# Optimization experiments

Hardware: AMD Instinct MI355X
Metric: run time of the kernel (lower is better)

Reference implementation:

```python
import jax, jax.numpy as jnp
import numpy as np

B, T, D = 2, 2048, 1024
F_DIM = 4096
E = 8


def setup_inputs() -> dict:
    key = jax.random.key(0)
    ks = jax.random.split(key, 6)
    x = jax.random.normal(ks[0], (B, T, D), dtype=jnp.float32)
    Wr = jax.random.normal(ks[1], (E, D), dtype=jnp.float32) * 0.02  # router weight [E, D]
    W1 = jax.random.normal(ks[2], (E, F_DIM, D), dtype=jnp.float32) * 0.02  # per-expert Linear(D->F) weights
    b1 = jnp.zeros((E, F_DIM), dtype=jnp.float32)
    W2 = jax.random.normal(ks[3], (E, D, F_DIM), dtype=jnp.float32) * 0.02  # per-expert Linear(F->D) weights
    b2 = jnp.zeros((E, D), dtype=jnp.float32)
    return {"x": x, "Wr": Wr, "W1": W1, "b1": b1, "W2": W2, "b2": b2, "top_k": 2}


def reference(x, Wr, W1, b1, W2, b2, top_k):
    # router scores: [b, t, E]
    scores = jnp.einsum('btd,ed->bte', x, Wr)
    topk_vals, topk_idx = jax.lax.top_k(scores, top_k)  # [b, t, k]
    # Dense compute over all experts (E is small); grouped-GEMM equivalent of the
    # original per-token loop. hidden: [b, t, E, F]
    h = jax.nn.relu(jnp.einsum('btd,efd->btef', x, W1) + b1)
    all_out = jnp.einsum('btef,edf->bted', h, W2) + b2  # [b, t, E, D]
    # gather the top-k experts' outputs per token: [b, t, k, D]
    gathered = jnp.take_along_axis(all_out, topk_idx[..., None], axis=2)
    # FAITHFUL to source: softmax over the sequence dim (dim=-1 of [b, t]),
    # applied independently per top-k slot.
    weight = jax.nn.softmax(topk_vals, axis=1)  # [b, t, k]
    out = jnp.sum(weight[..., None] * gathered, axis=2)  # [b, t, D]
    return out
```

## Files before the change

kernel.cpp:

```cpp
#include <hip/hip_runtime.h>
#include <stdint.h>

typedef short bf16x8 __attribute__((ext_vector_type(8)));
typedef float f32x4 __attribute__((ext_vector_type(4)));

#define NTOK 4096
#define DDIM 1024
#define FDIM 4096
#define NEXP 8
#define SEQ  2048

#define FB_MAXROWS 8704
#define FB_MAXTILES 136
#define N_MAXROWS 9216
#define N_MAXTILES 72

#define GLOAD16(g, l) __builtin_amdgcn_global_load_lds( \
    (const __attribute__((address_space(1))) unsigned int*)(const void*)(g), \
    (__attribute__((address_space(3))) unsigned int*)(l), 16, 0, 0)

__device__ __forceinline__ unsigned short f2bf(float f) {
    union { float f; unsigned int u; } v; v.f = f;
    unsigned int u = v.u;
    unsigned int r = (u + 0x7FFFu + ((u >> 16) & 1u)) >> 16;
    return (unsigned short)r;
}
__device__ __forceinline__ unsigned int pk2(float a, float b) {
    return (unsigned int)f2bf(a) | ((unsigned int)f2bf(b) << 16);
}

__global__ __launch_bounds__(256) void cvt_kernel(
    const float* __restrict__ src, unsigned short* __restrict__ dst, int n4)
{
    int i = blockIdx.x * 256 + threadIdx.x;
    const int stride = gridDim.x * 256;
    for (; i < n4; i += stride) {
        const float4 v = ((const float4*)src)[i];
        ushort4 o;
        o.x = f2bf(v.x); o.y = f2bf(v.y); o.z = f2bf(v.z); o.w = f2bf(v.w);
        ((ushort4*)dst)[i] = o;
    }
}

__global__ __launch_bounds__(256) void router_kernel(
    const float* __restrict__ x, const float* __restrict__ Wr,
    float* __restrict__ topk_vals, int* __restrict__ topk_idx,
    int* __restrict__ counts)
{
    const int wave = threadIdx.x >> 6;
    const int lane = threadIdx.x & 63;
    const int t = blockIdx.x * 4 + wave;
    const float4* xr = (const float4*)(x + (size_t)t * DDIM);

    float acc[NEXP];
#pragma unroll
    for (int e = 0; e < NEXP; ++e) acc[e] = 0.0f;

    for (int d = lane; d < DDIM / 4; d += 64) {
        const float4 xv = xr[d];
#pragma unroll
        for (int e = 0; e < NEXP; ++e) {
            const float4 wv = ((const float4*)(Wr + e * DDIM))[d];
            acc[e] = fmaf(xv.x, wv.x, acc[e]);
            acc[e] = fmaf(xv.y, wv.y, acc[e]);
            acc[e] = fmaf(xv.z, wv.z, acc[e]);
            acc[e] = fmaf(xv.w, wv.w, acc[e]);
        }
    }
#pragma unroll
    for (int e = 0; e < NEXP; ++e) {
        for (int off = 32; off > 0; off >>= 1)
            acc[e] += __shfl_xor(acc[e], off, 64);
    }
    if (lane == 0) {
        float best = -3.4e38f, second = -3.4e38f;
        int bi = 0, si = 0;
#pragma unroll
        for (int e = 0; e < NEXP; ++e) {
            const float s = acc[e];
            if (s > best) { second = best; si = bi; best = s; bi = e; }
            else if (s > second) { second = s; si = e; }
        }
        topk_vals[t * 2 + 0] = best;
        topk_vals[t * 2 + 1] = second;
        topk_idx[t * 2 + 0] = bi;
        topk_idx[t * 2 + 1] = si;
        atomicAdd(&counts[bi], 1);
        atomicAdd(&counts[si], 1);
    }
}

__global__ __launch_bounds__(256) void softmax_seq_kernel(
    const float* __restrict__ tv, float* __restrict__ weight)
{
    const int b = blockIdx.x >> 1;
    const int k = blockIdx.x & 1;
    const float* base = tv + (size_t)b * SEQ * 2 + k;
    float* wbase = weight + (size_t)b * SEQ * 2 + k;
    __shared__ float red[256];
    const int tid = threadIdx.x;

    float m = -3.4e38f;
    for (int t = tid; t < SEQ; t += 256) m = fmaxf(m, base[t * 2]);
    red[tid] = m; __syncthreads();
    for (int s = 128; s > 0; s >>= 1) {
        if (tid < s) red[tid] = fmaxf(red[tid], red[tid + s]);
        __syncthreads();
    }
    m = red[0];
    __syncthreads();

    float sum = 0.0f;
    for (int t = tid; t < SEQ; t += 256) sum += expf(base[t * 2] - m);
    red[tid] = sum; __syncthreads();
    for (int s = 128; s > 0; s >>= 1) {
        if (tid < s) red[tid] += red[tid + s];
        __syncthreads();
    }
    const float inv = 1.0f / red[0];
    for (int t = tid; t < SEQ; t += 256)
        wbase[t * 2] = expf(base[t * 2] - m) * inv;
}

__global__ void scan_kernel(const int* __restrict__ counts,
                            int* __restrict__ padOff, int* __restrict__ cursor,
                            int padBits)
{
    if (threadIdx.x == 0) {
        const int pad = (1 << padBits) - 1;
        int o = 0;
        for (int e = 0; e < NEXP; ++e) {
            padOff[e] = o;
            o += ((counts[e] + pad) >> padBits) << padBits;
        }
        padOff[NEXP] = o;
    }
    if (threadIdx.x < NEXP) cursor[threadIdx.x] = 0;
}

__global__ __launch_bounds__(256) void scatter_kernel(
    const int* __restrict__ topk_idx, const int* __restrict__ padOff,
    int* __restrict__ cursor, int* __restrict__ perm)
{
    const int t = blockIdx.x * 256 + threadIdx.x;
#pragma unroll
    for (int k = 0; k < 2; ++k) {
        const int e = topk_idx[t * 2 + k];
        const int pos = padOff[e] + atomicAdd(&cursor[e], 1);
        perm[pos] = t * 2 + k;
    }
}


__global__ __launch_bounds__(256) void gemm1_p(
    const unsigned short* __restrict__ Xb, const unsigned short* __restrict__ Wb,
    const float* __restrict__ b1, const int* __restrict__ perm,
    const int* __restrict__ padOff, unsigned short* __restrict__ h)
{
    const int bid = blockIdx.x;
    const int swz = (bid & 7) * (2304 / 8) + (bid >> 3);
    const int by = swz % N_MAXTILES;
    const int bx = swz / N_MAXTILES;
    const int row0 = by * 128;
    if (row0 >= padOff[NEXP]) return;
    int e = 0;
#pragma unroll
    for (int i = 1; i < NEXP; ++i) if (row0 >= padOff[i]) e = i;

    __shared__ unsigned short As[2][128 * 64];
    __shared__ unsigned short Bs[2][128 * 64];

    const int tid = threadIdx.x;
    const int w = tid >> 6, lane = tid & 63;
    const int wm = (w & 1) * 64, wn = (w >> 1) * 64;
    const int fr = lane & 15, kg = lane >> 4;
    const int col0 = bx * 128;

    const unsigned short* aSrc[4];
    const unsigned short* bSrc[4];
#pragma unroll
    for (int j = 0; j < 4; ++j) {
        const int r = w * 32 + j * 8 + (lane >> 3);
        const int pm = perm[row0 + r];
        const int tok = (pm >= 0) ? (pm >> 1) : 0;
        aSrc[j] = Xb + (size_t)tok * DDIM + (lane & 7) * 8;
        bSrc[j] = Wb + ((size_t)e * FDIM + col0 + r) * DDIM + (lane & 7) * 8;
    }

    f32x4 acc[4][4] = {};

#pragma unroll
    for (int j = 0; j < 4; ++j) {
        GLOAD16(aSrc[j], &As[0][(w * 4 + j) * 512]);
        GLOAD16(bSrc[j], &Bs[0][(w * 4 + j) * 512]);
    }
    __syncthreads();

    int cur = 0;
    for (int k0 = 0; k0 < DDIM; k0 += 64) {
        const int nk = k0 + 64;
        if (nk < DDIM) {
#pragma unroll
            for (int j = 0; j < 4; ++j) {
                GLOAD16(aSrc[j] + nk, &As[cur ^ 1][(w * 4 + j) * 512]);
                GLOAD16(bSrc[j] + nk, &Bs[cur ^ 1][(w * 4 + j) * 512]);
            }
        }
        const unsigned short* Ab = &As[cur][0];
        const unsigned short* Bb = &Bs[cur][0];
#pragma unroll
        for (int kk = 0; kk < 2; ++kk) {
            bf16x8 a[4], b[4];
#pragma unroll
            for (int m = 0; m < 4; ++m)
                a[m] = *(const bf16x8*)&Ab[(wm + m * 16 + fr) * 64 + kk * 32 + kg * 8];
#pragma unroll
            for (int n = 0; n < 4; ++n)
                b[n] = *(const bf16x8*)&Bb[(wn + n * 16 + fr) * 64 + kk * 32 + kg * 8];
#pragma unroll
            for (int m = 0; m < 4; ++m)
#pragma unroll
                for (int n = 0; n < 4; ++n)
                    acc[m][n] = __builtin_amdgcn_mfma_f32_16x16x32_bf16(a[m], b[n], acc[m][n], 0, 0, 0);
        }
        __syncthreads();
        cur ^= 1;
    }

#pragma unroll
    for (int n = 0; n < 4; ++n) {
        const int colg = col0 + wn + n * 16 + fr;
        const float bias = b1[e * FDIM + colg];
#pragma unroll
        for (int m = 0; m < 4; ++m) {
#pragma unroll
            for (int r = 0; r < 4; ++r) {
                const int rowg = row0 + wm + m * 16 + kg * 4 + r;
                h[(size_t)rowg * FDIM + colg] = f2bf(fmaxf(acc[m][n][r] + bias, 0.0f));
            }
        }
    }
}

__global__ __launch_bounds__(256) void gemm2_p(
    const unsigned short* __restrict__ h, const unsigned short* __restrict__ Wb,
    const float* __restrict__ b2, const int* __restrict__ perm,
    const int* __restrict__ padOff, const float* __restrict__ weight,
    float* __restrict__ out)
{
    const int bid = blockIdx.x;
    const int swz = (bid & 7) * (576 / 8) + (bid >> 3);
    const int by = swz % N_MAXTILES;
    const int bx = swz / N_MAXTILES;
    const int row0 = by * 128;
    if (row0 >= padOff[NEXP]) return;
    int e = 0;
#pragma unroll
    for (int i = 1; i < NEXP; ++i) if (row0 >= padOff[i]) e = i;

    __shared__ unsigned short As[2][128 * 64];
    __shared__ unsigned short Bs[2][128 * 64];

    const int tid = threadIdx.x;
    const int w = tid >> 6, lane = tid & 63;
    const int wm = (w & 1) * 64, wn = (w >> 1) * 64;
    const int fr = lane & 15, kg = lane >> 4;
    const int col0 = bx * 128;

    const unsigned short* aSrc[4];
    const unsigned short* bSrc[4];
#pragma unroll
    for (int j = 0; j < 4; ++j) {
        const int r = w * 32 + j * 8 + (lane >> 3);
        aSrc[j] = h + (size_t)(row0 + r) * FDIM + (lane & 7) * 8;
        bSrc[j] = Wb + ((size_t)e * DDIM + col0 + r) * FDIM + (lane & 7) * 8;
    }

    f32x4 acc[4][4] = {};

#pragma unroll
    for (int j = 0; j < 4; ++j) {
        GLOAD16(aSrc[j], &As[0][(w * 4 + j) * 512]);
        GLOAD16(bSrc[j], &Bs[0][(w * 4 + j) * 512]);
    }
    __syncthreads();

    int cur = 0;
    for (int k0 = 0; k0 < FDIM; k0 += 64) {
        const int nk = k0 + 64;
        if (nk < FDIM) {
#pragma unroll
            for (int j = 0; j < 4; ++j) {
                GLOAD16(aSrc[j] + nk, &As[cur ^ 1][(w * 4 + j) * 512]);
                GLOAD16(bSrc[j] + nk, &Bs[cur ^ 1][(w * 4 + j) * 512]);
            }
        }
        const unsigned short* Ab = &As[cur][0];
        const unsigned short* Bb = &Bs[cur][0];
#pragma unroll
        for (int kk = 0; kk < 2; ++kk) {
            bf16x8 a[4], b[4];
#pragma unroll
            for (int m = 0; m < 4; ++m)
                a[m] = *(const bf16x8*)&Ab[(wm + m * 16 + fr) * 64 + kk * 32 + kg * 8];
#pragma unroll
            for (int n = 0; n < 4; ++n)
                b[n] = *(const bf16x8*)&Bb[(wn + n * 16 + fr) * 64 + kk * 32 + kg * 8];
#pragma unroll
            for (int m = 0; m < 4; ++m)
#pragma unroll
                for (int n = 0; n < 4; ++n)
                    acc[m][n] = __builtin_amdgcn_mfma_f32_16x16x32_bf16(a[m], b[n], acc[m][n], 0, 0, 0);
        }
        __syncthreads();
        cur ^= 1;
    }

#pragma unroll
    for (int n = 0; n < 4; ++n) {
        const int colg = col0 + wn + n * 16 + fr;
        const float bias = b2[e * DDIM + colg];
#pragma unroll
        for (int m = 0; m < 4; ++m) {
#pragma unroll
            for (int r = 0; r < 4; ++r) {
                const int rowg = row0 + wm + m * 16 + kg * 4 + r;
                const int pm = perm[rowg];
                if (pm >= 0) {
                    const float wgt = weight[pm];
                    atomicAdd(&out[(size_t)(pm >> 1) * DDIM + colg], (acc[m][n][r] + bias) * wgt);
                }
            }
        }
    }
}


__global__ __launch_bounds__(256) void gemm1_fb(
    const float* __restrict__ x, const float* __restrict__ W1,
    const float* __restrict__ b1, const int* __restrict__ perm,
    const int* __restrict__ padOff, unsigned short* __restrict__ h)
{
    const int row0 = blockIdx.y * 64;
    if (row0 >= padOff[NEXP]) return;
    int e = 0;
#pragma unroll
    for (int i = 1; i < NEXP; ++i) if (row0 >= padOff[i]) e = i;

    __shared__ unsigned short As[64][40];
    __shared__ unsigned short Bs[64][40];

    const int tid = threadIdx.x;
    const int srow = tid >> 2;
    const int skp = (tid & 3) << 3;

    const int pm = perm[row0 + srow];
    const float* aSrc = (pm >= 0) ? (x + (size_t)(pm >> 1) * DDIM + skp) : 0;
    const int fRow = blockIdx.x * 64 + srow;
    const float* bSrc = W1 + ((size_t)e * FDIM + fRow) * DDIM + skp;

    const int lane = tid & 63;
    const int wm = ((tid >> 7) & 1) * 32;
    const int wn = ((tid >> 6) & 1) * 32;
    const int fr = lane & 15;
    const int kg = lane >> 4;

    f32x4 acc[2][2] = {{{0,0,0,0},{0,0,0,0}},{{0,0,0,0},{0,0,0,0}}};

    for (int k0 = 0; k0 < DDIM; k0 += 32) {
        uint4 av = make_uint4(0, 0, 0, 0);
        if (aSrc) {
            const float4 lo = *(const float4*)(aSrc + k0);
            const float4 hi = *(const float4*)(aSrc + k0 + 4);
            av.x = pk2(lo.x, lo.y); av.y = pk2(lo.z, lo.w);
            av.z = pk2(hi.x, hi.y); av.w = pk2(hi.z, hi.w);
        }
        const float4 bl = *(const float4*)(bSrc + k0);
        const float4 bh = *(const float4*)(bSrc + k0 + 4);
        uint4 bv;
        bv.x = pk2(bl.x, bl.y); bv.y = pk2(bl.z, bl.w);
        bv.z = pk2(bh.x, bh.y); bv.w = pk2(bh.z, bh.w);

        __syncthreads();
        *(uint4*)&As[srow][skp] = av;
        *(uint4*)&Bs[srow][skp] = bv;
        __syncthreads();

        const bf16x8 a0 = *(const bf16x8*)&As[wm + 0  + fr][kg << 3];
        const bf16x8 a1 = *(const bf16x8*)&As[wm + 16 + fr][kg << 3];
        const bf16x8 b0 = *(const bf16x8*)&Bs[wn + 0  + fr][kg << 3];
        const bf16x8 b1v = *(const bf16x8*)&Bs[wn + 16 + fr][kg << 3];
        acc[0][0] = __builtin_amdgcn_mfma_f32_16x16x32_bf16(a0, b0,  acc[0][0], 0, 0, 0);
        acc[0][1] = __builtin_amdgcn_mfma_f32_16x16x32_bf16(a0, b1v, acc[0][1], 0, 0, 0);
        acc[1][0] = __builtin_amdgcn_mfma_f32_16x16x32_bf16(a1, b0,  acc[1][0], 0, 0, 0);
        acc[1][1] = __builtin_amdgcn_mfma_f32_16x16x32_bf16(a1, b1v, acc[1][1], 0, 0, 0);
    }

#pragma unroll
    for (int mi = 0; mi < 2; ++mi)
#pragma unroll
        for (int ni = 0; ni < 2; ++ni) {
            const int colg = blockIdx.x * 64 + wn + ni * 16 + fr;
            const float bias = b1[e * FDIM + colg];
#pragma unroll
            for (int r = 0; r < 4; ++r) {
                const int rowg = row0 + wm + mi * 16 + (kg << 2) + r;
                float v = acc[mi][ni][r] + bias;
                v = fmaxf(v, 0.0f);
                h[(size_t)rowg * FDIM + colg] = f2bf(v);
            }
        }
}

__global__ __launch_bounds__(256) void gemm2_fb(
    const unsigned short* __restrict__ h, const float* __restrict__ W2,
    const float* __restrict__ b2, const int* __restrict__ perm,
    const int* __restrict__ padOff, const float* __restrict__ weight,
    float* __restrict__ out)
{
    const int row0 = blockIdx.y * 64;
    if (row0 >= padOff[NEXP]) return;
    int e = 0;
#pragma unroll
    for (int i = 1; i < NEXP; ++i) if (row0 >= padOff[i]) e = i;

    __shared__ unsigned short As[64][40];
    __shared__ unsigned short Bs[64][40];

    const int tid = threadIdx.x;
    const int srow = tid >> 2;
    const int skp = (tid & 3) << 3;

    const unsigned short* aSrc = h + (size_t)(row0 + srow) * FDIM + skp;
    const int dRow = blockIdx.x * 64 + srow;
    const float* bSrc = W2 + ((size_t)e * DDIM + dRow) * FDIM + skp;

    const int lane = tid & 63;
    const int wm = ((tid >> 7) & 1) * 32;
    const int wn = ((tid >> 6) & 1) * 32;
    const int fr = lane & 15;
    const int kg = lane >> 4;

    f32x4 acc[2][2] = {{{0,0,0,0},{0,0,0,0}},{{0,0,0,0},{0,0,0,0}}};

    for (int k0 = 0; k0 < FDIM; k0 += 32) {
        const uint4 av = *(const uint4*)(aSrc + k0);
        const float4 bl = *(const float4*)(bSrc + k0);
        const float4 bh = *(const float4*)(bSrc + k0 + 4);
        uint4 bv;
        bv.x = pk2(bl.x, bl.y); bv.y = pk2(bl.z, bl.w);
        bv.z = pk2(bh.x, bh.y); bv.w = pk2(bh.z, bh.w);

        __syncthreads();
        *(uint4*)&As[srow][skp] = av;
        *(uint4*)&Bs[srow][skp] = bv;
        __syncthreads();

        const bf16x8 a0 = *(const bf16x8*)&As[wm + 0  + fr][kg << 3];
        const bf16x8 a1 = *(const bf16x8*)&As[wm + 16 + fr][kg << 3];
        const bf16x8 b0 = *(const bf16x8*)&Bs[wn + 0  + fr][kg << 3];
        const bf16x8 b1v = *(const bf16x8*)&Bs[wn + 16 + fr][kg << 3];
        acc[0][0] = __builtin_amdgcn_mfma_f32_16x16x32_bf16(a0, b0,  acc[0][0], 0, 0, 0);
        acc[0][1] = __builtin_amdgcn_mfma_f32_16x16x32_bf16(a0, b1v, acc[0][1], 0, 0, 0);
        acc[1][0] = __builtin_amdgcn_mfma_f32_16x16x32_bf16(a1, b0,  acc[1][0], 0, 0, 0);
        acc[1][1] = __builtin_amdgcn_mfma_f32_16x16x32_bf16(a1, b1v, acc[1][1], 0, 0, 0);
    }

#pragma unroll
    for (int mi = 0; mi < 2; ++mi)
#pragma unroll
        for (int ni = 0; ni < 2; ++ni) {
            const int colg = blockIdx.x * 64 + wn + ni * 16 + fr;
            const float bias = b2[e * DDIM + colg];
#pragma unroll
            for (int r = 0; r < 4; ++r) {
                const int rowg = row0 + wm + mi * 16 + (kg << 2) + r;
                const int pm = perm[rowg];
                if (pm >= 0) {
                    const float w = weight[pm];
                    const float v = (acc[mi][ni][r] + bias) * w;
                    atomicAdd(&out[(size_t)(pm >> 1) * DDIM + colg], v);
                }
            }
        }
}

extern "C" void kernel_launch(void* const* d_in, const int* in_sizes, int n_in,
                              void* d_out, int out_size, void* d_ws, size_t ws_size,
                              hipStream_t stream)
{
    const float* x  = (const float*)d_in[0];
    const float* Wr = (const float*)d_in[1];
    const float* W1 = (const float*)d_in[2];
    const float* b1 = (const float*)d_in[3];
    const float* W2 = (const float*)d_in[4];
    const float* b2 = (const float*)d_in[5];
    float* out = (float*)d_out;
    char* ws = (char*)d_ws;

    float* topk_vals = (float*)(ws);
    float* weight    = (float*)(ws + 32768);
    int*   topk_idx  = (int*)(ws + 65536);
    int*   counts    = (int*)(ws + 98304);
    int*   padOff    = (int*)(ws + 98368);
    int*   cursor    = (int*)(ws + 98432);
    int*   perm      = (int*)(ws + 98496);

    const size_t NEED = 151257088ULL;

    if (ws_size >= NEED) {
        unsigned short* Xb = (unsigned short*)(ws + 262144);
        unsigned short* h  = (unsigned short*)(ws + 8650752);
        unsigned short* Wb = (unsigned short*)(ws + 84148224);

        hipMemsetAsync(counts, 0, NEXP * sizeof(int), stream);
        hipMemsetAsync(perm, 0xFF, N_MAXROWS * sizeof(int), stream);
        hipMemsetAsync(out, 0, (size_t)out_size * sizeof(float), stream);

        cvt_kernel<<<2048, 256, 0, stream>>>(x, Xb, NTOK * DDIM / 4);
        cvt_kernel<<<2048, 256, 0, stream>>>(W1, Wb, NEXP * FDIM * DDIM / 4);
        router_kernel<<<NTOK / 4, 256, 0, stream>>>(x, Wr, topk_vals, topk_idx, counts);
        softmax_seq_kernel<<<4, 256, 0, stream>>>(topk_vals, weight);
        scan_kernel<<<1, 64, 0, stream>>>(counts, padOff, cursor, 7);
        scatter_kernel<<<NTOK / 256, 256, 0, stream>>>(topk_idx, padOff, cursor, perm);

        gemm1_p<<<32 * N_MAXTILES, 256, 0, stream>>>(Xb, Wb, b1, perm, padOff, h);
        cvt_kernel<<<2048, 256, 0, stream>>>(W2, Wb, NEXP * DDIM * FDIM / 4);
        gemm2_p<<<8 * N_MAXTILES, 256, 0, stream>>>(h, Wb, b2, perm, padOff, weight, out);
    } else {
        unsigned short* h = (unsigned short*)(ws + 135168);

        hipMemsetAsync(counts, 0, NEXP * sizeof(int), stream);
        hipMemsetAsync(perm, 0xFF, FB_MAXROWS * sizeof(int), stream);
        hipMemsetAsync(out, 0, (size_t)out_size * sizeof(float), stream);

        router_kernel<<<NTOK / 4, 256, 0, stream>>>(x, Wr, topk_vals, topk_idx, counts);
        softmax_seq_kernel<<<4, 256, 0, stream>>>(topk_vals, weight);
        scan_kernel<<<1, 64, 0, stream>>>(counts, padOff, cursor, 6);
        scatter_kernel<<<NTOK / 256, 256, 0, stream>>>(topk_idx, padOff, cursor, perm);

        gemm1_fb<<<dim3(FDIM / 64, FB_MAXTILES), 256, 0, stream>>>(x, W1, b1, perm, padOff, h);
        gemm2_fb<<<dim3(DDIM / 64, FB_MAXTILES), 256, 0, stream>>>(h, W2, b2, perm, padOff, weight, out);
    }
}
```

Baseline: 585.3 us.

## Add XOR-swizzled LDS, two-stage prefetch pipeline, and split-K for grouped GEMMs

Both grouped GEMMs now use an XOR-swizzled LDS layout so the fragment reads avoid bank conflicts. They also replace the single-prefetch __syncthreads loop with a two-tiles-ahead prefetch controlled by explicit vmcnt/lgkmcnt waits and raw barriers. gemm2 additionally splits K in two, doubling its grid for more parallelism, with the bias added only by the first K chunk. The costs are more atomic adds to the output and fragile hand-written waitcnt logic.

```diff
diff --git a/kernel.cpp b/kernel.cpp
--- a/kernel.cpp
+++ b/kernel.cpp
@@ -18,6 +18,12 @@
 #define GLOAD16(g, l) __builtin_amdgcn_global_load_lds( \
     (const __attribute__((address_space(1))) unsigned int*)(const void*)(g), \
     (__attribute__((address_space(3))) unsigned int*)(l), 16, 0, 0)
+
+#define WAIT_LGKM0() asm volatile("s_waitcnt lgkmcnt(0)" ::: "memory")
+#define WAIT_VM8()   asm volatile("s_waitcnt vmcnt(8)" ::: "memory")
+#define WAIT_VM0()   asm volatile("s_waitcnt vmcnt(0)" ::: "memory")
+#define SBAR()       __builtin_amdgcn_s_barrier()
+#define SCHEDB()     __builtin_amdgcn_sched_barrier(0)
 
 __device__ __forceinline__ unsigned short f2bf(float f) {
     union { float f; unsigned int u; } v; v.f = f;
@@ -158,7 +164,7 @@
     const int* __restrict__ padOff, unsigned short* __restrict__ h)
 {
     const int bid = blockIdx.x;
-    const int swz = (bid & 7) * (2304 / 8) + (bid >> 3);
+    const int swz = (bid & 7) * 288 + (bid >> 3);
     const int by = swz % N_MAXTILES;
     const int bx = swz / N_MAXTILES;
     const int row0 = by * 128;
@@ -176,6 +182,8 @@
     const int fr = lane & 15, kg = lane >> 4;
     const int col0 = bx * 128;
 
+    const int gchunk = ((lane & 7) ^ (lane >> 3)) * 8;
+
     const unsigned short* aSrc[4];
     const unsigned short* bSrc[4];
 #pragma unroll
@@ -183,49 +191,55 @@
         const int r = w * 32 + j * 8 + (lane >> 3);
         const int pm = perm[row0 + r];
         const int tok = (pm >= 0) ? (pm >> 1) : 0;
-        aSrc[j] = Xb + (size_t)tok * DDIM + (lane & 7) * 8;
-        bSrc[j] = Wb + ((size_t)e * FDIM + col0 + r) * DDIM + (lane & 7) * 8;
+        aSrc[j] = Xb + (size_t)tok * DDIM + gchunk;
+        bSrc[j] = Wb + ((size_t)e * FDIM + col0 + r) * DDIM + gchunk;
     }
 
     f32x4 acc[4][4] = {};
 
-#pragma unroll
-    for (int j = 0; j < 4; ++j) {
-        GLOAD16(aSrc[j], &As[0][(w * 4 + j) * 512]);
-        GLOAD16(bSrc[j], &Bs[0][(w * 4 + j) * 512]);
-    }
-    __syncthreads();
+#define STAGE1(buf, koff) do { \
+    for (int j = 0; j < 4; ++j) { \
+        GLOAD16(aSrc[j] + (koff), &As[buf][(w * 4 + j) * 512]); \
+        GLOAD16(bSrc[j] + (koff), &Bs[buf][(w * 4 + j) * 512]); \
+    } } while (0)
+
+    const int NT = DDIM / 64;
+    STAGE1(0, 0);
+    STAGE1(1, 64);
+    SCHEDB(); WAIT_VM8(); SBAR(); SCHEDB();
 
     int cur = 0;
-    for (int k0 = 0; k0 < DDIM; k0 += 64) {
-        const int nk = k0 + 64;
-        if (nk < DDIM) {
-#pragma unroll
-            for (int j = 0; j < 4; ++j) {
-                GLOAD16(aSrc[j] + nk, &As[cur ^ 1][(w * 4 + j) * 512]);
-                GLOAD16(bSrc[j] + nk, &Bs[cur ^ 1][(w * 4 + j) * 512]);
-            }
-        }
+    for (int t = 0; t < NT; ++t) {
         const unsigned short* Ab = &As[cur][0];
         const unsigned short* Bb = &Bs[cur][0];
+        bf16x8 a[2][4], b[2][4];
 #pragma unroll
         for (int kk = 0; kk < 2; ++kk) {
-            bf16x8 a[4], b[4];
 #pragma unroll
             for (int m = 0; m < 4; ++m)
-                a[m] = *(const bf16x8*)&Ab[(wm + m * 16 + fr) * 64 + kk * 32 + kg * 8];
+                a[kk][m] = *(const bf16x8*)&Ab[(wm + m * 16 + fr) * 64 + (((kk << 2) | kg) ^ (fr & 7)) * 8];
 #pragma unroll
             for (int n = 0; n < 4; ++n)
-                b[n] = *(const bf16x8*)&Bb[(wn + n * 16 + fr) * 64 + kk * 32 + kg * 8];
+                b[kk][n] = *(const bf16x8*)&Bb[(wn + n * 16 + fr) * 64 + (((kk << 2) | kg) ^ (fr & 7)) * 8];
+        }
+        WAIT_LGKM0(); SCHEDB();
+        SBAR(); SCHEDB();
+        if (t + 2 < NT) STAGE1(cur, (t + 2) * 64);
+#pragma unroll
+        for (int kk = 0; kk < 2; ++kk)
 #pragma unroll
             for (int m = 0; m < 4; ++m)
 #pragma unroll
                 for (int n = 0; n < 4; ++n)
-                    acc[m][n] = __builtin_amdgcn_mfma_f32_16x16x32_bf16(a[m], b[n], acc[m][n], 0, 0, 0);
-        }
-        __syncthreads();
+                    acc[m][n] = __builtin_amdgcn_mfma_f32_16x16x32_bf16(a[kk][m], b[kk][n], acc[m][n], 0, 0, 0);
+        if (t + 1 < NT) {
+            SCHEDB();
+            if (t + 2 < NT) { WAIT_VM8(); } else { WAIT_VM0(); }
+            SBAR(); SCHEDB();
+        }
         cur ^= 1;
     }
+#undef STAGE1
 
 #pragma unroll
     for (int n = 0; n < 4; ++n) {
@@ -249,9 +263,11 @@
     float* __restrict__ out)
 {
     const int bid = blockIdx.x;
-    const int swz = (bid & 7) * (576 / 8) + (bid >> 3);
+    const int swz = (bid & 7) * 144 + (bid >> 3);
     const int by = swz % N_MAXTILES;
-    const int bx = swz / N_MAXTILES;
+    const int rest = swz / N_MAXTILES;
+    const int bx = rest & 7;
+    const int kc = rest >> 3;
     const int row0 = by * 128;
     if (row0 >= padOff[NEXP]) return;
     int e = 0;
@@ -266,60 +282,69 @@
     const int wm = (w & 1) * 64, wn = (w >> 1) * 64;
     const int fr = lane & 15, kg = lane >> 4;
     const int col0 = bx * 128;
+    const int kbase = kc * (FDIM / 2);
+
+    const int gchunk = ((lane & 7) ^ (lane >> 3)) * 8;
 
     const unsigned short* aSrc[4];
     const unsigned short* bSrc[4];
 #pragma unroll
     for (int j = 0; j < 4; ++j) {
         const int r = w * 32 + j * 8 + (lane >> 3);
-        aSrc[j] = h + (size_t)(row0 + r) * FDIM + (lane & 7) * 8;
-        bSrc[j] = Wb + ((size_t)e * DDIM + col0 + r) * FDIM + (lane & 7) * 8;
+        aSrc[j] = h + (size_t)(row0 + r) * FDIM + kbase + gchunk;
+        bSrc[j] = Wb + ((size_t)e * DDIM + col0 + r) * FDIM + kbase + gchunk;
     }
 
     f32x4 acc[4][4] = {};
 
-#pragma unroll
-    for (int j = 0; j < 4; ++j) {
-        GLOAD16(aSrc[j], &As[0][(w * 4 + j) * 512]);
-        GLOAD16(bSrc[j], &Bs[0][(w * 4 + j) * 512]);
-    }
-    __syncthreads();
+#define STAGE2(buf, koff) do { \
+    for (int j = 0; j < 4; ++j) { \
+        GLOAD16(aSrc[j] + (koff), &As[buf][(w * 4 + j) * 512]); \
+        GLOAD16(bSrc[j] + (koff), &Bs[buf][(w * 4 + j) * 512]); \
+    } } while (0)
+
+    const int NT = (FDIM / 2) / 64;
+    STAGE2(0, 0);
+    STAGE2(1, 64);
+    SCHEDB(); WAIT_VM8(); SBAR(); SCHEDB();
 
     int cur = 0;
-    for (int k0 = 0; k0 < FDIM; k0 += 64) {
-        const int nk = k0 + 64;
-        if (nk < FDIM) {
-#pragma unroll
-            for (int j = 0; j < 4; ++j) {
-                GLOAD16(aSrc[j] + nk, &As[cur ^ 1][(w * 4 + j) * 512]);
-                GLOAD16(bSrc[j] + nk, &Bs[cur ^ 1][(w * 4 + j) * 512]);
-            }
-        }
+    for (int t = 0; t < NT; ++t) {
         const unsigned short* Ab = &As[cur][0];
         const unsigned short* Bb = &Bs[cur][0];
+        bf16x8 a[2][4], b[2][4];
 #pragma unroll
         for (int kk = 0; kk < 2; ++kk) {
-            bf16x8 a[4], b[4];
 #pragma unroll
             for (int m = 0; m < 4; ++m)
-                a[m] = *(const bf16x8*)&Ab[(wm + m * 16 + fr) * 64 + kk * 32 + kg * 8];
+                a[kk][m] = *(const bf16x8*)&Ab[(wm + m * 16 + fr) * 64 + (((kk << 2) | kg) ^ (fr & 7)) * 8];
 #pragma unroll
             for (int n = 0; n < 4; ++n)
-                b[n] = *(const bf16x8*)&Bb[(wn + n * 16 + fr) * 64 + kk * 32 + kg * 8];
+                b[kk][n] = *(const bf16x8*)&Bb[(wn + n * 16 + fr) * 64 + (((kk << 2) | kg) ^ (fr & 7)) * 8];
+        }
+        WAIT_LGKM0(); SCHEDB();
+        SBAR(); SCHEDB();
+        if (t + 2 < NT) STAGE2(cur, (t + 2) * 64);
+#pragma unroll
+        for (int kk = 0; kk < 2; ++kk)
 #pragma unroll
             for (int m = 0; m < 4; ++m)
 #pragma unroll
                 for (int n = 0; n < 4; ++n)
-                    acc[m][n] = __builtin_amdgcn_mfma_f32_16x16x32_bf16(a[m], b[n], acc[m][n], 0, 0, 0);
-        }
-        __syncthreads();
+                    acc[m][n] = __builtin_amdgcn_mfma_f32_16x16x32_bf16(a[kk][m], b[kk][n], acc[m][n], 0, 0, 0);
+        if (t + 1 < NT) {
+            SCHEDB();
+            if (t + 2 < NT) { WAIT_VM8(); } else { WAIT_VM0(); }
+            SBAR(); SCHEDB();
+        }
         cur ^= 1;
     }
+#undef STAGE2
 
 #pragma unroll
     for (int n = 0; n < 4; ++n) {
         const int colg = col0 + wn + n * 16 + fr;
-        const float bias = b2[e * DDIM + colg];
+        const float bias = (kc == 0) ? b2[e * DDIM + colg] : 0.0f;
 #pragma unroll
         for (int m = 0; m < 4; ++m) {
 #pragma unroll
@@ -526,7 +551,7 @@
 
         gemm1_p<<<32 * N_MAXTILES, 256, 0, stream>>>(Xb, Wb, b1, perm, padOff, h);
         cvt_kernel<<<2048, 256, 0, stream>>>(W2, Wb, NEXP * DDIM * FDIM / 4);
-        gemm2_p<<<8 * N_MAXTILES, 256, 0, stream>>>(h, Wb, b2, perm, padOff, weight, out);
+        gemm2_p<<<16 * N_MAXTILES, 256, 0, stream>>>(h, Wb, b2, perm, padOff, weight, out);
     } else {
         unsigned short* h = (unsigned short*)(ws + 135168);
 
```

New measurement: 524.3 us. -10.4%, faster.
